# Kernel optimization log

Measured on AMD Instinct MI355X. Metric: run time of the kernel, lower is better.

The kernel has to match this reference:

```python
import jax, jax.numpy as jnp
import numpy as np

K = 20  # hard-coded in LPDNet


def act(v):
    # LeakyReLU with negative_slope=0.0 == ReLU
    return jnp.maximum(v, 0.0)


def conv1d(x, w, b):
    # x: (B,C,N), w: (O,C), b: (O,) -> (B,O,N)  (1x1 Conv1d)
    return jnp.einsum('bcn,oc->bon', x, w) + b[None, :, None]


def conv2d(x, w, b):
    # x: (B,C,N,K), w: (O,C), b: (O,) -> (B,O,N,K)  (1x1 Conv2d)
    return jnp.einsum('bcnk,oc->bonk', x, w) + b[None, :, None, None]


def knn(x, k):
    # x: (B,C,N) -> idx (B,N,k) of nearest neighbors by negative squared L2
    xx = jnp.sum(x * x, axis=1)                       # (B,N)
    inner = jnp.einsum('bcn,bcm->bnm', x, x)          # (B,N,N)
    pairwise = 2.0 * inner - xx[:, :, None] - xx[:, None, :]
    _, idx = jax.lax.top_k(pairwise, k)
    return idx


def graph_feature(x, idx):
    # x: (B,C,N), idx: (B,N,k) -> (B,2C,N,k) as concat(neighbor - center, center)
    xt = jnp.transpose(x, (0, 2, 1))                  # (B,N,C)
    nbr = jax.vmap(lambda f, i: f[i])(xt, idx)        # (B,N,k,C)
    ctr = jnp.broadcast_to(xt[:, :, None, :], nbr.shape)
    feat = jnp.concatenate([nbr - ctr, ctr], axis=-1)  # (B,N,k,2C)
    return jnp.transpose(feat, (0, 3, 1, 2))          # (B,2C,N,k)


def setup_inputs():
    key = jax.random.key(0)
    ks = jax.random.split(key, 13)
    p = lambda k, s: jax.random.normal(k, s, jnp.float32) * 0.02
    return {
        'x': jax.random.normal(ks[0], (8, 1, 4096, 3), jnp.float32),
        'w1': p(ks[1], (64, 3)),    'b1': p(ks[2], (64,)),
        'w2': p(ks[3], (64, 64)),   'b2': p(ks[4], (64,)),
        'wdg1': p(ks[5], (128, 128)), 'bdg1': p(ks[6], (128,)),
        'wdg2': p(ks[7], (128, 128)), 'bdg2': p(ks[8], (128,)),
        'wsn1': p(ks[9], (256, 256)), 'bsn1': p(ks[10], (256,)),
        'w3': p(ks[11], (1024, 512)), 'b3': p(ks[12], (1024,)),
    }


def reference(x, w1, b1, w2, b2, wdg1, bdg1, wdg2, bdg2, wsn1, bsn1, w3, b3):
    xp = jnp.transpose(jnp.squeeze(x, 1), (0, 2, 1))  # (B,3,N)
    xinit = xp
    h = act(conv1d(xp, w1, b1))                       # (B,64,N)
    h = act(conv1d(h, w2, b2))                        # (B,64,N)
    idx1 = knn(h, K)
    g = graph_feature(h, idx1)                        # (B,128,N,K)
    g = act(conv2d(g, wdg1, bdg1))                    # (B,128,N,K)
    x1 = jnp.max(g, axis=-1)                          # (B,128,N)
    g = act(conv2d(g, wdg2, bdg2))                    # (B,128,N,K)
    x2 = jnp.max(g, axis=-1)                          # (B,128,N)
    idx2 = knn(xinit, K)                              # knn on raw 3D coords
    g = graph_feature(x2, idx2)                       # (B,256,N,K)
    g = act(conv2d(g, wsn1, bsn1))                    # (B,256,N,K)
    x3 = jnp.max(g, axis=-1)                          # (B,256,N)
    cat = jnp.concatenate([x1, x2, x3], axis=1)       # (B,512,N)
    out = act(conv1d(cat, w3, b3))                    # (B,1024,N)
    return out[..., None]                             # (B,1024,N,1)
```

## Files before the change

### kernel.cpp

```cpp
#include <hip/hip_runtime.h>
#include <stdint.h>


#define NB 8
#define NP 4096
#define NPTS (NB*NP)

typedef float  floatx4 __attribute__((ext_vector_type(4)));
typedef short  short8  __attribute__((ext_vector_type(8)));

__device__ __forceinline__ unsigned short f2bf(float f) {
  union { float f; uint32_t u; } v; v.f = f;
  uint32_t r = v.u + 0x7fffu + ((v.u >> 16) & 1u);
  return (unsigned short)(r >> 16);
}
__device__ __forceinline__ float bf2f(unsigned short h) {
  union { uint32_t u; float f; } v; v.u = ((uint32_t)h) << 16;
  return v.f;
}

__device__ __forceinline__ floatx4 mfma_bf16(short8 a, short8 b, floatx4 c) {
  return __builtin_amdgcn_mfma_f32_16x16x32_bf16(a, b, c, 0, 0, 0);
}

__global__ void cvt_weights(const float* wdg1, unsigned short* wdg1b,
                            const float* wdg2, unsigned short* wdg2b,
                            const float* wsn1, unsigned short* wsn1b,
                            const float* w3, unsigned short* w3b) {
  int i = blockIdx.x * 256 + threadIdx.x;
  if (i < 16384) {
    int c = i & 127;
    wdg1b[i] = f2bf(wdg1[i] - (c >= 64 ? wdg1[i - 64] : 0.f));
  }
  if (i < 16384) wdg2b[i] = f2bf(wdg2[i]);
  if (i < 65536) {
    int c = i & 255;
    wsn1b[i] = f2bf(wsn1[i] - (c >= 128 ? wsn1[i - 128] : 0.f));
  }
  if (i < 524288) w3b[i] = f2bf(w3[i]);
}

__global__ __launch_bounds__(256) void conv12(
    const float* __restrict__ xin, const float* __restrict__ w1,
    const float* __restrict__ b1, const float* __restrict__ w2,
    const float* __restrict__ b2,
    unsigned short* __restrict__ hb16, unsigned short* __restrict__ hlo16,
    float* __restrict__ hh, float* __restrict__ cc) {
  int wave = threadIdx.x >> 6, lane = threadIdx.x & 63;
  int p = blockIdx.x * 4 + wave;
  __shared__ float s_h1[4][64];
  const float* xp = xin + p * 3;
  float c0 = xp[0], c1 = xp[1], c2 = xp[2];
  float v = b1[lane] + w1[lane*3+0]*c0 + w1[lane*3+1]*c1 + w1[lane*3+2]*c2;
  s_h1[wave][lane] = fmaxf(v, 0.f);
  __syncthreads();
  float acc = b2[lane];
  const float* wr = w2 + lane * 64;
  #pragma unroll
  for (int c = 0; c < 64; c += 4) {
    floatx4 w4 = *(const floatx4*)(wr + c);
    acc += w4[0]*s_h1[wave][c]   + w4[1]*s_h1[wave][c+1]
         + w4[2]*s_h1[wave][c+2] + w4[3]*s_h1[wave][c+3];
  }
  acc = fmaxf(acc, 0.f);
  unsigned short hi = f2bf(acc);
  hb16[p*64 + lane] = hi;
  hlo16[p*64 + lane] = f2bf(acc - bf2f(hi));
  float sq = acc * acc;
  #pragma unroll
  for (int off = 32; off; off >>= 1) sq += __shfl_xor(sq, off, 64);
  if (lane == 0) { hh[p] = sq; cc[p] = c0*c0 + c1*c1 + c2*c2; }
}

__global__ __launch_bounds__(256) void knn64_mfma(
    const unsigned short* __restrict__ Hhi, const unsigned short* __restrict__ Hlo,
    const float* __restrict__ XX, int* __restrict__ idx_out) {
  __shared__ unsigned short mhi[128][72];
  __shared__ unsigned short mlo[128][72];
  __shared__ float dots[64][132];
  __shared__ float xxMh[128];
  __shared__ float tau[64];
  int b = blockIdx.y;
  int r0 = blockIdx.x * 64;
  int t = threadIdx.x;
  int lane = t & 63, wave = t >> 6;
  int quad = lane >> 4, l15 = lane & 15;
  const unsigned short* Hhib = Hhi + (size_t)b * NP * 64;
  const unsigned short* Hlob = Hlo + (size_t)b * NP * 64;
  short8 ahi[2], alo[2];
  {
    const unsigned short* pr = Hhib + (size_t)(r0 + wave * 16 + l15) * 64 + quad * 8;
    const unsigned short* pl = Hlob + (size_t)(r0 + wave * 16 + l15) * 64 + quad * 8;
    ahi[0] = *(const short8*)pr; ahi[1] = *(const short8*)(pr + 32);
    alo[0] = *(const short8*)pl; alo[1] = *(const short8*)(pl + 32);
  }
  if (t < 64) tau[t] = -__builtin_inff();

  float lv[20]; int li[20];
  #pragma unroll
  for (int s = 0; s < 20; s++) { lv[s] = -__builtin_inff(); li[s] = 0x7fffffff; }
  float minval = -__builtin_inff(); int minpos = 0;
  int row = t >> 2, sub = t & 3;

  for (int mt = 0; mt < NP / 128; mt++) {
    int m0 = mt * 128;
    {
      int hf = t & 1, r = (t >> 1) & 127;
      int c0 = hf * 32;
      const unsigned short* sh = Hhib + (size_t)(m0 + r) * 64 + c0;
      const unsigned short* sl = Hlob + (size_t)(m0 + r) * 64 + c0;
      *(short8*)&mhi[r][c0]      = *(const short8*)sh;
      *(short8*)&mhi[r][c0 + 8]  = *(const short8*)(sh + 8);
      *(short8*)&mhi[r][c0 + 16] = *(const short8*)(sh + 16);
      *(short8*)&mhi[r][c0 + 24] = *(const short8*)(sh + 24);
      *(short8*)&mlo[r][c0]      = *(const short8*)sl;
      *(short8*)&mlo[r][c0 + 8]  = *(const short8*)(sl + 8);
      *(short8*)&mlo[r][c0 + 16] = *(const short8*)(sl + 16);
      *(short8*)&mlo[r][c0 + 24] = *(const short8*)(sl + 24);
    }
    if (t < 128) xxMh[t] = 0.5f * XX[b * NP + m0 + t];
    __syncthreads();
    #pragma unroll
    for (int nt = 0; nt < 8; nt++) {
      floatx4 acc = (floatx4)0.f;
      #pragma unroll
      for (int ks = 0; ks < 2; ks++) {
        int k0 = ks * 32 + quad * 8;
        short8 bhi = *(short8*)&mhi[nt * 16 + l15][k0];
        short8 blo = *(short8*)&mlo[nt * 16 + l15][k0];
        acc = mfma_bf16(ahi[ks], bhi, acc);
        acc = mfma_bf16(ahi[ks], blo, acc);
        acc = mfma_bf16(alo[ks], bhi, acc);
        acc = mfma_bf16(alo[ks], blo, acc);
      }
      int colg = nt * 16 + l15;
      float xm = xxMh[colg];
      #pragma unroll
      for (int r = 0; r < 4; r++) {
        int mr = wave * 16 + quad * 4 + r;
        dots[mr][colg] = acc[r] - xm;
      }
    }
    __syncthreads();
    float gate = fmaxf(minval, tau[row]);
    floatx4 dv[8];
    #pragma unroll
    for (int q = 0; q < 8; q++) dv[q] = *(floatx4*)&dots[row][sub * 32 + q * 4];
    uint32_t mask = 0;
    #pragma unroll
    for (int q = 0; q < 8; q++)
      #pragma unroll
      for (int j = 0; j < 4; j++)
        if (dv[q][j] > gate) mask |= 1u << (q * 4 + j);
    #pragma clang loop unroll(disable)
    for (int round = 0; round < 32; round++) {
      if (!__any(mask != 0)) break;
      if (mask) {
        int i = __builtin_ctz(mask); mask &= mask - 1;
        float v = dots[row][sub * 32 + i];
        if (v > minval) {
          int gi = m0 + sub * 32 + i;
          #pragma unroll
          for (int s = 0; s < 20; s++)
            if (s == minpos) { lv[s] = v; li[s] = gi; }
          minval = __builtin_inff();
          #pragma unroll
          for (int s = 0; s < 20; s++)
            if (lv[s] < minval) { minval = lv[s]; minpos = s; }
        }
      }
    }
    tau[row] = fmaxf(tau[row], minval);
  }
  int base = (b * NP + r0 + row) * 20;
  for (int sel = 0; sel < 20; sel++) {
    float mybv = -__builtin_inff(); int mybi = 0x7fffffff, mybs = 0;
    #pragma unroll
    for (int s = 0; s < 20; s++) {
      bool better = lv[s] > mybv || (lv[s] == mybv && li[s] < mybi);
      if (better) { mybv = lv[s]; mybi = li[s]; mybs = s; }
    }
    float bv = mybv; int bi = mybi;
    float ov = __shfl_xor(bv, 1, 64); int oi = __shfl_xor(bi, 1, 64);
    if (ov > bv || (ov == bv && oi < bi)) { bv = ov; bi = oi; }
    ov = __shfl_xor(bv, 2, 64); oi = __shfl_xor(bi, 2, 64);
    if (ov > bv || (ov == bv && oi < bi)) { bv = ov; bi = oi; }
    if (sub == 0) idx_out[base + sel] = bi;
    if (bi == mybi) {
      #pragma unroll
      for (int s = 0; s < 20; s++)
        if (s == mybs) { lv[s] = -__builtin_inff(); li[s] = 0x7fffffff; }
    }
  }
}

template<int C>
__global__ __launch_bounds__(256) void knn_topk(
    const float* __restrict__ X, const float* __restrict__ XX,
    int* __restrict__ idx_out) {
  __shared__ float rowsT[C][68];
  __shared__ float mT[C][68];
  __shared__ float dots[64][68];
  __shared__ float xxMh[64];
  __shared__ float tau[64];
  int b = blockIdx.y;
  int r0 = blockIdx.x * 64;
  int t = threadIdx.x;
  const float* Xb = X + (size_t)b * NP * C;
  for (int e = t; e < C * 64; e += 256) {
    int r = e / C, c = e - r * C;
    rowsT[c][r] = Xb[(r0 + r) * C + c];
  }
  if (t < 64) tau[t] = -__builtin_inff();

  float lv[20]; int li[20];
  #pragma unroll
  for (int s = 0; s < 20; s++) { lv[s] = -__builtin_inff(); li[s] = 0x7fffffff; }
  float minval = -__builtin_inff(); int minpos = 0;

  int tm = t & 15, tr = t >> 4;
  int row = t >> 2, sub = t & 3;

  for (int mt = 0; mt < NP / 64; mt++) {
    int m0 = mt * 64;
    for (int e = t; e < C * 64; e += 256) {
      int r = e / C, c = e - r * C;
      mT[c][r] = Xb[(m0 + r) * C + c];
    }
    if (t < 64) xxMh[t] = 0.5f * XX[b * NP + m0 + t];
    __syncthreads();
    float acc[4][4];
    #pragma unroll
    for (int i = 0; i < 4; i++)
      #pragma unroll
      for (int j = 0; j < 4; j++) acc[i][j] = 0.f;
    for (int c = 0; c < C; c++) {
      floatx4 av = *(floatx4*)&rowsT[c][tr * 4];
      floatx4 bv = *(floatx4*)&mT[c][tm * 4];
      #pragma unroll
      for (int i = 0; i < 4; i++)
        #pragma unroll
        for (int j = 0; j < 4; j++) acc[i][j] += av[i] * bv[j];
    }
    #pragma unroll
    for (int i = 0; i < 4; i++) {
      floatx4 sv;
      #pragma unroll
      for (int j = 0; j < 4; j++)
        sv[j] = acc[i][j] - xxMh[tm*4 + j];
      *(floatx4*)&dots[tr*4 + i][tm*4] = sv;
    }
    __syncthreads();
    float gate = fmaxf(minval, tau[row]);
    floatx4 dv0 = *(floatx4*)&dots[row][sub * 16];
    floatx4 dv1 = *(floatx4*)&dots[row][sub * 16 + 4];
    floatx4 dv2 = *(floatx4*)&dots[row][sub * 16 + 8];
    floatx4 dv3 = *(floatx4*)&dots[row][sub * 16 + 12];
    uint32_t mask = 0;
    #pragma unroll
    for (int j = 0; j < 4; j++) {
      if (dv0[j] > gate) mask |= 1u << j;
      if (dv1[j] > gate) mask |= 1u << (4 + j);
      if (dv2[j] > gate) mask |= 1u << (8 + j);
      if (dv3[j] > gate) mask |= 1u << (12 + j);
    }
    #pragma clang loop unroll(disable)
    for (int round = 0; round < 16; round++) {
      if (!__any(mask != 0)) break;
      if (mask) {
        int i = __builtin_ctz(mask); mask &= mask - 1;
        float v = dots[row][sub * 16 + i];
        if (v > minval) {
          int gi = m0 + sub * 16 + i;
          #pragma unroll
          for (int s = 0; s < 20; s++)
            if (s == minpos) { lv[s] = v; li[s] = gi; }
          minval = __builtin_inff();
          #pragma unroll
          for (int s = 0; s < 20; s++)
            if (lv[s] < minval) { minval = lv[s]; minpos = s; }
        }
      }
    }
    tau[row] = fmaxf(tau[row], minval);
  }
  int base = (b * NP + r0 + row) * 20;
  for (int sel = 0; sel < 20; sel++) {
    float mybv = -__builtin_inff(); int mybi = 0x7fffffff, mybs = 0;
    #pragma unroll
    for (int s = 0; s < 20; s++) {
      bool better = lv[s] > mybv || (lv[s] == mybv && li[s] < mybi);
      if (better) { mybv = lv[s]; mybi = li[s]; mybs = s; }
    }
    float bv = mybv; int bi = mybi;
    float ov = __shfl_xor(bv, 1, 64); int oi = __shfl_xor(bi, 1, 64);
    if (ov > bv || (ov == bv && oi < bi)) { bv = ov; bi = oi; }
    ov = __shfl_xor(bv, 2, 64); oi = __shfl_xor(bi, 2, 64);
    if (ov > bv || (ov == bv && oi < bi)) { bv = ov; bi = oi; }
    if (sub == 0) idx_out[base + sel] = bi;
    if (bi == mybi) {
      #pragma unroll
      for (int s = 0; s < 20; s++)
        if (s == mybs) { lv[s] = -__builtin_inff(); li[s] = 0x7fffffff; }
    }
  }
}

__global__ __launch_bounds__(256) void dg_stage(
    const unsigned short* __restrict__ hb16, const int* __restrict__ idx1,
    const unsigned short* __restrict__ w1b, const float* __restrict__ bia1,
    const unsigned short* __restrict__ w2b, const float* __restrict__ bia2,
    unsigned short* __restrict__ featb) {
  __shared__ unsigned short s_a[80][136];
  __shared__ unsigned short s_v[80][136];
  __shared__ int s_nbf[80];
  int p0 = blockIdx.x * 4;
  int b = p0 >> 12, n0 = p0 & 4095;
  int t = threadIdx.x;
  int lane = t & 63, wave = t >> 6;
  if (t < 80) s_nbf[t] = idx1[p0 * 20 + t];
  __syncthreads();
  const unsigned short* hbb = hb16 + (size_t)b * NP * 64;
  {
    int cc = (t & 15) * 8;
    int r00 = t >> 4;
    #pragma unroll
    for (int it = 0; it < 5; it++) {
      int row = r00 + it * 16;
      const unsigned short* src = (cc < 64)
        ? hbb + (size_t)s_nbf[row] * 64 + cc
        : hbb + (size_t)(n0 + row / 20) * 64 + (cc - 64);
      *(short8*)&s_a[row][cc] = *(const short8*)src;
    }
  }
  __syncthreads();
  int quad = lane >> 4, mrow = lane & 15;
  int nblock = wave * 32;
  {
    floatx4 acc[5][2];
    #pragma unroll
    for (int mt = 0; mt < 5; mt++) { acc[mt][0] = (floatx4)0.f; acc[mt][1] = (floatx4)0.f; }
    #pragma unroll
    for (int ks = 0; ks < 4; ks++) {
      int k0 = ks * 32 + quad * 8;
      short8 w0 = *(const short8*)(w1b + (nblock + mrow) * 128 + k0);
      short8 w1v = *(const short8*)(w1b + (nblock + 16 + mrow) * 128 + k0);
      #pragma unroll
      for (int mt = 0; mt < 5; mt++) {
        short8 a = *(short8*)&s_a[mt * 16 + mrow][k0];
        acc[mt][0] = mfma_bf16(a, w0, acc[mt][0]);
        acc[mt][1] = mfma_bf16(a, w1v, acc[mt][1]);
      }
    }
    #pragma unroll
    for (int ns = 0; ns < 2; ns++) {
      int o = nblock + ns * 16 + mrow;
      float bz = bia1[o];
      #pragma unroll
      for (int mt = 0; mt < 5; mt++)
        #pragma unroll
        for (int r = 0; r < 4; r++)
          s_v[mt * 16 + quad * 4 + r][o] = f2bf(fmaxf(acc[mt][ns][r] + bz, 0.f));
    }
  }
  __syncthreads();
  #pragma unroll
  for (int it = 0; it < 2; it++) {
    int e = t + it * 256;
    int pt = e >> 7, o = e & 127;
    float mx = 0.f;
    for (int k = 0; k < 20; k++) mx = fmaxf(mx, bf2f(s_v[pt * 20 + k][o]));
    featb[(size_t)(p0 + pt) * 512 + o] = f2bf(mx);
  }
  {
    floatx4 acc[5][2];
    #pragma unroll
    for (int mt = 0; mt < 5; mt++) { acc[mt][0] = (floatx4)0.f; acc[mt][1] = (floatx4)0.f; }
    #pragma unroll
    for (int ks = 0; ks < 4; ks++) {
      int k0 = ks * 32 + quad * 8;
      short8 w0 = *(const short8*)(w2b + (nblock + mrow) * 128 + k0);
      short8 w1v = *(const short8*)(w2b + (nblock + 16 + mrow) * 128 + k0);
      #pragma unroll
      for (int mt = 0; mt < 5; mt++) {
        short8 a = *(short8*)&s_v[mt * 16 + mrow][k0];
        acc[mt][0] = mfma_bf16(a, w0, acc[mt][0]);
        acc[mt][1] = mfma_bf16(a, w1v, acc[mt][1]);
      }
    }
    #pragma unroll
    for (int ns = 0; ns < 2; ns++) {
      int o = nblock + ns * 16 + mrow;
      float bz = bia2[o];
      #pragma unroll
      for (int mt = 0; mt < 5; mt++)
        #pragma unroll
        for (int r = 0; r < 4; r++)
          s_a[mt * 16 + quad * 4 + r][o] = f2bf(fmaxf(acc[mt][ns][r] + bz, 0.f));
    }
  }
  __syncthreads();
  #pragma unroll
  for (int it = 0; it < 2; it++) {
    int e = t + it * 256;
    int pt = e >> 7, o = e & 127;
    float mx = 0.f;
    for (int k = 0; k < 20; k++) mx = fmaxf(mx, bf2f(s_a[pt * 20 + k][o]));
    featb[(size_t)(p0 + pt) * 512 + 128 + o] = f2bf(mx);
  }
}

__global__ __launch_bounds__(256) void sn_stage(
    const int* __restrict__ idx2, const unsigned short* __restrict__ wb,
    const float* __restrict__ bias, unsigned short* __restrict__ featb) {
  __shared__ unsigned short s_a[80][264];
  __shared__ int s_nbf[80];
  int p0 = blockIdx.x * 4;
  int b = p0 >> 12, n0 = p0 & 4095;
  int bb = b << 12;
  int t = threadIdx.x;
  int lane = t & 63, wave = t >> 6;
  if (t < 80) s_nbf[t] = idx2[p0 * 20 + t];
  __syncthreads();
  {
    int cc = (t & 31) * 8;
    int r00 = t >> 5;
    #pragma unroll
    for (int it = 0; it < 10; it++) {
      int row = r00 + it * 8;
      const unsigned short* src = (cc < 128)
        ? featb + (size_t)(bb + s_nbf[row]) * 512 + 128 + cc
        : featb + (size_t)(bb + n0 + row / 20) * 512 + cc;
      *(short8*)&s_a[row][cc] = *(const short8*)src;
    }
  }
  __syncthreads();
  int quad = lane >> 4, mrow = lane & 15;
  int nblock = wave * 64;
  floatx4 acc[5][4];
  #pragma unroll
  for (int mt = 0; mt < 5; mt++)
    #pragma unroll
    for (int ns = 0; ns < 4; ns++) acc[mt][ns] = (floatx4)0.f;
  #pragma unroll
  for (int ks = 0; ks < 8; ks++) {
    int k0 = ks * 32 + quad * 8;
    short8 w[4];
    #pragma unroll
    for (int ns = 0; ns < 4; ns++)
      w[ns] = *(const short8*)(wb + (nblock + ns * 16 + mrow) * 256 + k0);
    #pragma unroll
    for (int mt = 0; mt < 5; mt++) {
      short8 a = *(short8*)&s_a[mt * 16 + mrow][k0];
      #pragma unroll
      for (int ns = 0; ns < 4; ns++)
        acc[mt][ns] = mfma_bf16(a, w[ns], acc[mt][ns]);
    }
  }
  __syncthreads();
  #pragma unroll
  for (int ns = 0; ns < 4; ns++) {
    int o = nblock + ns * 16 + mrow;
    float bz = bias[o];
    #pragma unroll
    for (int mt = 0; mt < 5; mt++)
      #pragma unroll
      for (int r = 0; r < 4; r++)
        s_a[mt * 16 + quad * 4 + r][o] = f2bf(fmaxf(acc[mt][ns][r] + bz, 0.f));
  }
  __syncthreads();
  #pragma unroll
  for (int it = 0; it < 4; it++) {
    int e = t + it * 256;
    int pt = e >> 8, o = e & 255;
    float mx = 0.f;
    for (int k = 0; k < 20; k++) mx = fmaxf(mx, bf2f(s_a[pt * 20 + k][o]));
    featb[(size_t)(p0 + pt) * 512 + 256 + o] = f2bf(mx);
  }
}

__global__ __launch_bounds__(256) void conv3_gemm(
    const unsigned short* __restrict__ w3b, const unsigned short* __restrict__ featb,
    const float* __restrict__ b3, float* __restrict__ out) {
  __shared__ unsigned short s_a[128][40];
  __shared__ unsigned short s_b[128][40];
  int o0 = blockIdx.x * 128, p0 = blockIdx.y * 128;
  int t = threadIdx.x, lane = t & 63, wave = t >> 6;
  int wy = wave >> 1, wx = wave & 1;
  int quad = lane >> 4, l15 = lane & 15;
  floatx4 acc[4][4];
  #pragma unroll
  for (int i = 0; i < 4; i++)
    #pragma unroll
    for (int j = 0; j < 4; j++) acc[i][j] = (floatx4)0.f;
  for (int kc = 0; kc < 16; kc++) {
    __syncthreads();
    for (int e = t; e < 512; e += 256) {
      int r = e >> 2, c8 = (e & 3) * 8;
      *(short8*)&s_a[r][c8] = *(const short8*)(w3b + (size_t)(o0 + r) * 512 + kc * 32 + c8);
    }
    for (int e = t; e < 512; e += 256) {
      int r = e >> 2, c8 = (e & 3) * 8;
      *(short8*)&s_b[r][c8] = *(const short8*)(featb + (size_t)(p0 + r) * 512 + kc * 32 + c8);
    }
    __syncthreads();
    int k0 = quad * 8;
    short8 af[4], bfr[4];
    #pragma unroll
    for (int i = 0; i < 4; i++) af[i] = *(short8*)&s_a[wy * 64 + i * 16 + l15][k0];
    #pragma unroll
    for (int j = 0; j < 4; j++) bfr[j] = *(short8*)&s_b[wx * 64 + j * 16 + l15][k0];
    #pragma unroll
    for (int i = 0; i < 4; i++)
      #pragma unroll
      for (int j = 0; j < 4; j++) acc[i][j] = mfma_bf16(af[i], bfr[j], acc[i][j]);
  }
  #pragma unroll
  for (int i = 0; i < 4; i++)
    #pragma unroll
    for (int j = 0; j < 4; j++) {
      int pl = p0 + wx * 64 + j * 16 + l15;
      int bI = pl >> 12, n = pl & 4095;
      #pragma unroll
      for (int r = 0; r < 4; r++) {
        int o = o0 + wy * 64 + i * 16 + quad * 4 + r;
        out[(size_t)(bI * 1024 + o) * 4096 + n] = fmaxf(acc[i][j][r] + b3[o], 0.f);
      }
    }
}

extern "C" void kernel_launch(void* const* d_in, const int* in_sizes, int n_in,
                              void* d_out, int out_size, void* d_ws, size_t ws_size,
                              hipStream_t stream) {
  const float* x    = (const float*)d_in[0];
  const float* w1   = (const float*)d_in[1];
  const float* b1   = (const float*)d_in[2];
  const float* w2   = (const float*)d_in[3];
  const float* b2   = (const float*)d_in[4];
  const float* wdg1 = (const float*)d_in[5];
  const float* bdg1 = (const float*)d_in[6];
  const float* wdg2 = (const float*)d_in[7];
  const float* bdg2 = (const float*)d_in[8];
  const float* wsn1 = (const float*)d_in[9];
  const float* bsn1 = (const float*)d_in[10];
  const float* w3   = (const float*)d_in[11];
  const float* b3   = (const float*)d_in[12];

  float* ws = (float*)d_ws;
  unsigned short* hlo16 = (unsigned short*)ws;
  float* hh = ws + 2097152;
  float* cc = ws + 2129920;
  int* idx1 = (int*)(ws + 2162688);
  int* idx2 = (int*)(ws + 2818048);
  unsigned short* featb = (unsigned short*)(ws + 3473408);
  unsigned short* wdg1b = (unsigned short*)(ws + 11862016);
  unsigned short* wdg2b = (unsigned short*)(ws + 11870208);
  unsigned short* wsn1b = (unsigned short*)(ws + 11878400);
  unsigned short* w3b   = (unsigned short*)(ws + 11911168);
  unsigned short* hb16  = (unsigned short*)(ws + 12173312);

  cvt_weights<<<2048, 256, 0, stream>>>(wdg1, wdg1b, wdg2, wdg2b,
                                        wsn1, wsn1b, w3, w3b);
  conv12<<<8192, 256, 0, stream>>>(x, w1, b1, w2, b2, hb16, hlo16, hh, cc);
  knn64_mfma<<<dim3(64, 8), 256, 0, stream>>>(hb16, hlo16, hh, idx1);
  knn_topk<3><<<dim3(64, 8), 256, 0, stream>>>(x, cc, idx2);
  dg_stage<<<8192, 256, 0, stream>>>(hb16, idx1, wdg1b, bdg1, wdg2b, bdg2, featb);
  sn_stage<<<8192, 256, 0, stream>>>(idx2, wsn1b, bsn1, featb);
  conv3_gemm<<<dim3(8, 256), 256, 0, stream>>>(w3b, featb, b3, (float*)d_out);
}
```

Measured before the change: 1.033 ms.

## Fuse both KNN kernels into one launch sharing LDS, swap tile widths

Merges the 64-channel MFMA KNN and the 3D-coordinate KNN into one kernel whose blocks alternate between the two workloads over a shared LDS buffer. The aim is to run both searches concurrently, fill the GPU with 1024 blocks instead of two serial 512-block launches, and remove one launch gap. The column tile widths are also swapped: the MFMA path moves to 64-column tiles and the 3D path to 128-column tiles. This changes the per-tile top-k scan granularity and register pressure, and the fused kernel's occupancy is bounded by the heavier of the two bodies.

Result: slower. 1.062 ms (+2.8%).

```diff
diff --git a/kernel.cpp b/kernel.cpp
--- a/kernel.cpp
+++ b/kernel.cpp
@@ -72,16 +72,18 @@
   if (lane == 0) { hh[p] = sq; cc[p] = c0*c0 + c1*c1 + c2*c2; }
 }
 
-__global__ __launch_bounds__(256) void knn64_mfma(
+
+__device__ __forceinline__ void knn64_body(
+    unsigned char* smem,
     const unsigned short* __restrict__ Hhi, const unsigned short* __restrict__ Hlo,
-    const float* __restrict__ XX, int* __restrict__ idx_out) {
-  __shared__ unsigned short mhi[128][72];
-  __shared__ unsigned short mlo[128][72];
-  __shared__ float dots[64][132];
-  __shared__ float xxMh[128];
-  __shared__ float tau[64];
-  int b = blockIdx.y;
-  int r0 = blockIdx.x * 64;
+    const float* __restrict__ XX, int* __restrict__ idx_out,
+    int xt, int b) {
+  auto mhi  = (unsigned short (*)[72])(smem);
+  auto mlo  = (unsigned short (*)[72])(smem + 9216);
+  auto dots = (float (*)[68])(smem + 18432);
+  float* xxMh = (float*)(smem + 35840);
+  float* tau  = (float*)(smem + 36096);
+  int r0 = xt * 64;
   int t = threadIdx.x;
   int lane = t & 63, wave = t >> 6;
   int quad = lane >> 4, l15 = lane & 15;
@@ -102,26 +104,21 @@
   float minval = -__builtin_inff(); int minpos = 0;
   int row = t >> 2, sub = t & 3;
 
-  for (int mt = 0; mt < NP / 128; mt++) {
-    int m0 = mt * 128;
+  for (int mt = 0; mt < NP / 64; mt++) {
+    int m0 = mt * 64;
     {
-      int hf = t & 1, r = (t >> 1) & 127;
-      int c0 = hf * 32;
-      const unsigned short* sh = Hhib + (size_t)(m0 + r) * 64 + c0;
-      const unsigned short* sl = Hlob + (size_t)(m0 + r) * 64 + c0;
-      *(short8*)&mhi[r][c0]      = *(const short8*)sh;
-      *(short8*)&mhi[r][c0 + 8]  = *(const short8*)(sh + 8);
-      *(short8*)&mhi[r][c0 + 16] = *(const short8*)(sh + 16);
-      *(short8*)&mhi[r][c0 + 24] = *(const short8*)(sh + 24);
-      *(short8*)&mlo[r][c0]      = *(const short8*)sl;
-      *(short8*)&mlo[r][c0 + 8]  = *(const short8*)(sl + 8);
-      *(short8*)&mlo[r][c0 + 16] = *(const short8*)(sl + 16);
-      *(short8*)&mlo[r][c0 + 24] = *(const short8*)(sl + 24);
-    }
-    if (t < 128) xxMh[t] = 0.5f * XX[b * NP + m0 + t];
+      int pt = t >> 2, c0 = (t & 3) * 16;
+      const unsigned short* sh = Hhib + (size_t)(m0 + pt) * 64 + c0;
+      const unsigned short* sl = Hlob + (size_t)(m0 + pt) * 64 + c0;
+      *(short8*)&mhi[pt][c0]     = *(const short8*)sh;
+      *(short8*)&mhi[pt][c0 + 8] = *(const short8*)(sh + 8);
+      *(short8*)&mlo[pt][c0]     = *(const short8*)sl;
+      *(short8*)&mlo[pt][c0 + 8] = *(const short8*)(sl + 8);
+    }
+    if (t < 64) xxMh[t] = 0.5f * XX[b * NP + m0 + t];
     __syncthreads();
     #pragma unroll
-    for (int nt = 0; nt < 8; nt++) {
+    for (int nt = 0; nt < 4; nt++) {
       floatx4 acc = (floatx4)0.f;
       #pragma unroll
       for (int ks = 0; ks < 2; ks++) {
@@ -140,6 +137,125 @@
         int mr = wave * 16 + quad * 4 + r;
         dots[mr][colg] = acc[r] - xm;
       }
+    }
+    __syncthreads();
+    float gate = fmaxf(minval, tau[row]);
+    floatx4 dv0 = *(floatx4*)&dots[row][sub * 16];
+    floatx4 dv1 = *(floatx4*)&dots[row][sub * 16 + 4];
+    floatx4 dv2 = *(floatx4*)&dots[row][sub * 16 + 8];
+    floatx4 dv3 = *(floatx4*)&dots[row][sub * 16 + 12];
+    uint32_t mask = 0;
+    #pragma unroll
+    for (int j = 0; j < 4; j++) {
+      if (dv0[j] > gate) mask |= 1u << j;
+      if (dv1[j] > gate) mask |= 1u << (4 + j);
+      if (dv2[j] > gate) mask |= 1u << (8 + j);
+      if (dv3[j] > gate) mask |= 1u << (12 + j);
+    }
+    #pragma clang loop unroll(disable)
+    for (int round = 0; round < 16; round++) {
+      if (!__any(mask != 0)) break;
+      if (mask) {
+        int i = __builtin_ctz(mask); mask &= mask - 1;
+        float v = dots[row][sub * 16 + i];
+        if (v > minval) {
+          int gi = m0 + sub * 16 + i;
+          #pragma unroll
+          for (int s = 0; s < 20; s++)
+            if (s == minpos) { lv[s] = v; li[s] = gi; }
+          minval = __builtin_inff();
+          #pragma unroll
+          for (int s = 0; s < 20; s++)
+            if (lv[s] < minval) { minval = lv[s]; minpos = s; }
+        }
+      }
+    }
+    tau[row] = fmaxf(tau[row], minval);
+  }
+  int base = (b * NP + r0 + row) * 20;
+  for (int sel = 0; sel < 20; sel++) {
+    float mybv = -__builtin_inff(); int mybi = 0x7fffffff, mybs = 0;
+    #pragma unroll
+    for (int s = 0; s < 20; s++) {
+      bool better = lv[s] > mybv || (lv[s] == mybv && li[s] < mybi);
+      if (better) { mybv = lv[s]; mybi = li[s]; mybs = s; }
+    }
+    float bv = mybv; int bi = mybi;
+    float ov = __shfl_xor(bv, 1, 64); int oi = __shfl_xor(bi, 1, 64);
+    if (ov > bv || (ov == bv && oi < bi)) { bv = ov; bi = oi; }
+    ov = __shfl_xor(bv, 2, 64); oi = __shfl_xor(bi, 2, 64);
+    if (ov > bv || (ov == bv && oi < bi)) { bv = ov; bi = oi; }
+    if (sub == 0) idx_out[base + sel] = bi;
+    if (bi == mybi) {
+      #pragma unroll
+      for (int s = 0; s < 20; s++)
+        if (s == mybs) { lv[s] = -__builtin_inff(); li[s] = 0x7fffffff; }
+    }
+  }
+}
+
+__device__ __forceinline__ void knn3_body(
+    unsigned char* smem,
+    const float* __restrict__ X, const float* __restrict__ XX,
+    int* __restrict__ idx_out, int xt, int b) {
+  constexpr int C = 3;
+  auto rowsT = (float (*)[68])(smem);
+  auto mT    = (float (*)[132])(smem + 816);
+  auto dots  = (float (*)[132])(smem + 2400);
+  float* xxMh = (float*)(smem + 36192);
+  float* tau  = (float*)(smem + 36704);
+  int r0 = xt * 64;
+  int t = threadIdx.x;
+  const float* Xb = X + (size_t)b * NP * C;
+  for (int e = t; e < C * 64; e += 256) {
+    int r = e / C, c = e - r * C;
+    rowsT[c][r] = Xb[(r0 + r) * C + c];
+  }
+  if (t < 64) tau[t] = -__builtin_inff();
+
+  float lv[20]; int li[20];
+  #pragma unroll
+  for (int s = 0; s < 20; s++) { lv[s] = -__builtin_inff(); li[s] = 0x7fffffff; }
+  float minval = -__builtin_inff(); int minpos = 0;
+
+  int tm = t & 15, tr = t >> 4;
+  int row = t >> 2, sub = t & 3;
+
+  for (int mt = 0; mt < NP / 128; mt++) {
+    int m0 = mt * 128;
+    for (int e = t; e < C * 128; e += 256) {
+      int r = e / C, c = e - r * C;
+      mT[c][r] = Xb[(m0 + r) * C + c];
+    }
+    if (t < 128) xxMh[t] = 0.5f * XX[b * NP + m0 + t];
+    __syncthreads();
+    float acc[4][8];
+    #pragma unroll
+    for (int i = 0; i < 4; i++)
+      #pragma unroll
+      for (int j = 0; j < 8; j++) acc[i][j] = 0.f;
+    for (int c = 0; c < C; c++) {
+      floatx4 av  = *(floatx4*)&rowsT[c][tr * 4];
+      floatx4 bv0 = *(floatx4*)&mT[c][tm * 8];
+      floatx4 bv1 = *(floatx4*)&mT[c][tm * 8 + 4];
+      #pragma unroll
+      for (int i = 0; i < 4; i++)
+        #pragma unroll
+        for (int j = 0; j < 4; j++) {
+          acc[i][j]     += av[i] * bv0[j];
+          acc[i][j + 4] += av[i] * bv1[j];
+        }
+    }
+    #pragma unroll
+    for (int i = 0; i < 4; i++) {
+      floatx4 sv0, sv1;
+      #pragma unroll
+      for (int j = 0; j < 4; j++) {
+        sv0[j] = acc[i][j]     - xxMh[tm*8 + j];
+        sv1[j] = acc[i][j + 4] - xxMh[tm*8 + 4 + j];
+      }
+      *(floatx4*)&dots[tr*4 + i][tm*8]     = sv0;
+      *(floatx4*)&dots[tr*4 + i][tm*8 + 4] = sv1;
     }
     __syncthreads();
     float gate = fmaxf(minval, tau[row]);
@@ -194,116 +310,18 @@
   }
 }
 
-template<int C>
-__global__ __launch_bounds__(256) void knn_topk(
-    const float* __restrict__ X, const float* __restrict__ XX,
-    int* __restrict__ idx_out) {
-  __shared__ float rowsT[C][68];
-  __shared__ float mT[C][68];
-  __shared__ float dots[64][68];
-  __shared__ float xxMh[64];
-  __shared__ float tau[64];
+__global__ __launch_bounds__(256) void knn_fused(
+    const unsigned short* __restrict__ Hhi, const unsigned short* __restrict__ Hlo,
+    const float* __restrict__ HH,
+    const float* __restrict__ X, const float* __restrict__ CC,
+    int* __restrict__ idx1, int* __restrict__ idx2) {
+  __shared__ __attribute__((aligned(16))) unsigned char smem[36960];
+  int xt = blockIdx.x >> 1;
   int b = blockIdx.y;
-  int r0 = blockIdx.x * 64;
-  int t = threadIdx.x;
-  const float* Xb = X + (size_t)b * NP * C;
-  for (int e = t; e < C * 64; e += 256) {
-    int r = e / C, c = e - r * C;
-    rowsT[c][r] = Xb[(r0 + r) * C + c];
-  }
-  if (t < 64) tau[t] = -__builtin_inff();
-
-  float lv[20]; int li[20];
-  #pragma unroll
-  for (int s = 0; s < 20; s++) { lv[s] = -__builtin_inff(); li[s] = 0x7fffffff; }
-  float minval = -__builtin_inff(); int minpos = 0;
-
-  int tm = t & 15, tr = t >> 4;
-  int row = t >> 2, sub = t & 3;
-
-  for (int mt = 0; mt < NP / 64; mt++) {
-    int m0 = mt * 64;
-    for (int e = t; e < C * 64; e += 256) {
-      int r = e / C, c = e - r * C;
-      mT[c][r] = Xb[(m0 + r) * C + c];
-    }
-    if (t < 64) xxMh[t] = 0.5f * XX[b * NP + m0 + t];
-    __syncthreads();
-    float acc[4][4];
-    #pragma unroll
-    for (int i = 0; i < 4; i++)
-      #pragma unroll
-      for (int j = 0; j < 4; j++) acc[i][j] = 0.f;
-    for (int c = 0; c < C; c++) {
-      floatx4 av = *(floatx4*)&rowsT[c][tr * 4];
-      floatx4 bv = *(floatx4*)&mT[c][tm * 4];
-      #pragma unroll
-      for (int i = 0; i < 4; i++)
-        #pragma unroll
-        for (int j = 0; j < 4; j++) acc[i][j] += av[i] * bv[j];
-    }
-    #pragma unroll
-    for (int i = 0; i < 4; i++) {
-      floatx4 sv;
-      #pragma unroll
-      for (int j = 0; j < 4; j++)
-        sv[j] = acc[i][j] - xxMh[tm*4 + j];
-      *(floatx4*)&dots[tr*4 + i][tm*4] = sv;
-    }
-    __syncthreads();
-    float gate = fmaxf(minval, tau[row]);
-    floatx4 dv0 = *(floatx4*)&dots[row][sub * 16];
-    floatx4 dv1 = *(floatx4*)&dots[row][sub * 16 + 4];
-    floatx4 dv2 = *(floatx4*)&dots[row][sub * 16 + 8];
-    floatx4 dv3 = *(floatx4*)&dots[row][sub * 16 + 12];
-    uint32_t mask = 0;
-    #pragma unroll
-    for (int j = 0; j < 4; j++) {
-      if (dv0[j] > gate) mask |= 1u << j;
-      if (dv1[j] > gate) mask |= 1u << (4 + j);
-      if (dv2[j] > gate) mask |= 1u << (8 + j);
-      if (dv3[j] > gate) mask |= 1u << (12 + j);
-    }
-    #pragma clang loop unroll(disable)
-    for (int round = 0; round < 16; round++) {
-      if (!__any(mask != 0)) break;
-      if (mask) {
-        int i = __builtin_ctz(mask); mask &= mask - 1;
-        float v = dots[row][sub * 16 + i];
-        if (v > minval) {
-          int gi = m0 + sub * 16 + i;
-          #pragma unroll
-          for (int s = 0; s < 20; s++)
-            if (s == minpos) { lv[s] = v; li[s] = gi; }
-          minval = __builtin_inff();
-          #pragma unroll
-          for (int s = 0; s < 20; s++)
-            if (lv[s] < minval) { minval = lv[s]; minpos = s; }
-        }
-      }
-    }
-    tau[row] = fmaxf(tau[row], minval);
-  }
-  int base = (b * NP + r0 + row) * 20;
-  for (int sel = 0; sel < 20; sel++) {
-    float mybv = -__builtin_inff(); int mybi = 0x7fffffff, mybs = 0;
-    #pragma unroll
-    for (int s = 0; s < 20; s++) {
-      bool better = lv[s] > mybv || (lv[s] == mybv && li[s] < mybi);
-      if (better) { mybv = lv[s]; mybi = li[s]; mybs = s; }
-    }
-    float bv = mybv; int bi = mybi;
-    float ov = __shfl_xor(bv, 1, 64); int oi = __shfl_xor(bi, 1, 64);
-    if (ov > bv || (ov == bv && oi < bi)) { bv = ov; bi = oi; }
-    ov = __shfl_xor(bv, 2, 64); oi = __shfl_xor(bi, 2, 64);
-    if (ov > bv || (ov == bv && oi < bi)) { bv = ov; bi = oi; }
-    if (sub == 0) idx_out[base + sel] = bi;
-    if (bi == mybi) {
-      #pragma unroll
-      for (int s = 0; s < 20; s++)
-        if (s == mybs) { lv[s] = -__builtin_inff(); li[s] = 0x7fffffff; }
-    }
-  }
+  if ((blockIdx.x & 1) == 0)
+    knn64_body(smem, Hhi, Hlo, HH, idx1, xt, b);
+  else
+    knn3_body(smem, X, CC, idx2, xt, b);
 }
 
 __global__ __launch_bounds__(256) void dg_stage(
@@ -562,8 +580,7 @@
   cvt_weights<<<2048, 256, 0, stream>>>(wdg1, wdg1b, wdg2, wdg2b,
                                         wsn1, wsn1b, w3, w3b);
   conv12<<<8192, 256, 0, stream>>>(x, w1, b1, w2, b2, hb16, hlo16, hh, cc);
-  knn64_mfma<<<dim3(64, 8), 256, 0, stream>>>(hb16, hlo16, hh, idx1);
-  knn_topk<3><<<dim3(64, 8), 256, 0, stream>>>(x, cc, idx2);
+  knn_fused<<<dim3(128, 8), 256, 0, stream>>>(hb16, hlo16, hh, x, cc, idx1, idx2);
   dg_stage<<<8192, 256, 0, stream>>>(hb16, idx1, wdg1b, bdg1, wdg2b, bdg2, featb);
   sn_stage<<<8192, 256, 0, stream>>>(idx2, wsn1b, bsn1, featb);
   conv3_gemm<<<dim3(8, 256), 256, 0, stream>>>(w3b, featb, b3, (float*)d_out);
```
